# Kernel tuning notes

Measured on AMD Instinct MI355X. Metric: run time of the kernel, lower is better.

Reference implementation:

```python
import jax, jax.numpy as jnp
import numpy as np

B, D, K = 32, 256, 128
DIM, DEPTH, HEADS, MULT, NF = 512, 4, 8, 4, 4
TAU = 0.1
HD = DIM // HEADS  # head_dim = 64


def rms_norm(x, eps=1e-6):
    return x * jax.lax.rsqrt(jnp.mean(x * x, axis=-1, keepdims=True) + eps)


def apply_rope(x, cos, sin):
    # x: (B, S, H, hd); cos/sin: (S, hd//2); interleaved (re, im) pairs
    c = cos[None, :, None, :]
    s = sin[None, :, None, :]
    xr = x[..., 0::2]
    xi = x[..., 1::2]
    out = jnp.stack([xr * c - xi * s, xr * s + xi * c], axis=-1)
    return out.reshape(x.shape)


def one_hot_minus(inputs, shift):
    # (inputs - shift) % K in one-hot space; shift_matrix[u, v] = shift[(v - u) % K]
    Kv = inputs.shape[-1]
    idx = (jnp.arange(Kv)[None, :] - jnp.arange(Kv)[:, None]) % Kv  # (K, K)
    shift_mat = shift[..., idx]  # (..., K, K) axes (u, v)
    return jnp.einsum('...v,...uv->...u', inputs, shift_mat)


def attention(x, qkvW, oW, cos, sin):
    Bx, S, _ = x.shape
    qkv = x @ qkvW.T
    q, k, v = jnp.split(qkv, [HEADS * HD, 2 * HEADS * HD], axis=-1)
    q = rms_norm(q.reshape(Bx, S, HEADS, HD))
    k = rms_norm(k.reshape(Bx, S, HEADS, HD))
    v = v.reshape(Bx, S, HEADS, HD)
    q = apply_rope(q, cos, sin)
    k = apply_rope(k, cos, sin)
    scores = jnp.einsum('bqhd,bkhd->bhqk', q, k) * (1.0 / HD ** 0.5)
    a = jax.nn.softmax(scores, axis=-1)
    o = jnp.einsum('bhqk,bkhd->bqhd', a, v).reshape(Bx, S, DIM)
    return o @ oW.T


def mlp(x, upW, downW):
    h = jax.nn.relu(x @ upW.T)
    return (h * h) @ downW.T


def setup_inputs():
    key = jax.random.key(0)
    ks = jax.random.split(key, 12)
    f = lambda k, sh, sc: jax.random.normal(k, sh, dtype=jnp.float32) * sc
    return {
        'y': jax.random.randint(ks[0], (B, D), 0, K, dtype=jnp.int32),
        'base_logits': f(ks[1], (D, K), 0.02),
        'embed_W': f(ks[2], (NF, DIM, K), 0.05),
        'pos_embed': f(ks[3], (NF, D, DIM), 0.02),
        'qkv_W': f(ks[4], (NF, DEPTH, (HEADS + 2 * HEADS) * HD, DIM), 0.02),
        'out_W': f(ks[5], (NF, DEPTH, DIM, DIM), 0.02),
        'up_W': f(ks[6], (NF, DEPTH, DIM * MULT, DIM), 0.02),
        'down_W': f(ks[7], (NF, DEPTH, DIM, DIM * MULT), 0.02),
        'skip_alpha': jnp.zeros((NF, DEPTH // 2), jnp.float32),
        'head_W': f(ks[8], (NF, K, DIM), 0.02),
        'head_b': jnp.zeros((NF, K), jnp.float32),
    }


def reference(y, base_logits, embed_W, pos_embed, qkv_W, out_W, up_W, down_W,
              skip_alpha, head_W, head_b):
    # RoPE cache over D positions
    dpa = HD // 2
    inv_freq = 1.0 / (10000.0 ** (jnp.arange(dpa, dtype=jnp.float32) / dpa))
    ang = jnp.arange(D, dtype=jnp.float32)[:, None] * inv_freq[None, :]
    cos, sin = jnp.cos(ang), jnp.sin(ang)
    even = (jnp.arange(D) % 2 == 0).astype(jnp.float32)[:, None]  # (D, 1)

    def coupling_net(xin, i):
        h = xin @ embed_W[i].T + pos_embed[i][None]
        mid = DEPTH // 2
        skips = []
        for b in range(DEPTH):
            if mid > 0 and b >= mid:
                h = h + jax.nn.sigmoid(skip_alpha[i, b - mid]) * skips.pop()
            h = h + attention(rms_norm(h), qkv_W[i, b], out_W[i, b], cos, sin)
            h = h + mlp(rms_norm(h), up_W[i, b], down_W[i, b])
            if mid > 0 and b < mid:
                skips.append(h)
        return rms_norm(h) @ head_W[i].T + head_b[i]

    x = jax.nn.one_hot(y, K, dtype=jnp.float32)  # (B, D, K)
    for i in reversed(range(NF)):
        mask = even if i % 2 == 0 else 1.0 - even
        logits = coupling_net(mask * x, i)
        soft = jax.nn.softmax(logits / TAU, axis=-1)
        hard = jax.nn.one_hot(jnp.argmax(logits, axis=-1), K, dtype=jnp.float32)
        loc = soft + jax.lax.stop_gradient(hard - soft)  # straight-through one-hot
        x = mask * x + (1.0 - mask) * one_hot_minus(x, loc)
    log_base = jax.nn.log_softmax(base_logits, axis=-1)
    return jnp.sum(log_base[None] * x, axis=(-1, -2))  # (B,)
```

## Files before the change

kernel.cpp:

```cpp
#include <hip/hip_runtime.h>

typedef __attribute__((ext_vector_type(8))) short s16x8;
typedef __attribute__((ext_vector_type(4))) float f32x4;

#define B_ 32
#define D_ 256
#define K_ 128
#define DIM_ 512
#define HEADS_ 8
#define HD_ 64
#define S_ 256
#define TOK_ (B_*D_)

__device__ __forceinline__ unsigned short f2bf(float f) {
    union { float f; unsigned int u; } v; v.f = f;
    unsigned int r = v.u + 0x7fffu + ((v.u >> 16) & 1u);
    return (unsigned short)(r >> 16);
}
__device__ __forceinline__ float bf2f(unsigned short u) {
    union { unsigned int u; float f; } v; v.u = ((unsigned int)u) << 16;
    return v.f;
}

typedef const __attribute__((address_space(1))) unsigned int* gp1_t;
typedef __attribute__((address_space(3))) unsigned int* lp3_t;
__device__ __forceinline__ void gload16(const void* g, void* l) {
    __builtin_amdgcn_global_load_lds((gp1_t)g, (lp3_t)l, 16, 0, 0);
}

template<int BM, int BN, int EPI, bool SWZ>
__global__ __launch_bounds__(256)
void gemm_p(const unsigned short* __restrict__ A, const unsigned short* __restrict__ Bw,
            void* __restrict__ Cv, const float* __restrict__ bias,
            int K, int ldc, long sA, long sB, int zdiv, long sC1, long sC2)
{
    constexpr int FM = BM/32, FN = BN/32;
    constexpr int AP = BM*4/256, BP = BN*4/256;
    __shared__ unsigned short As[2][BM*32];
    __shared__ unsigned short Bs[2][BN*32];

    const int tid = threadIdx.x;
    const int z = blockIdx.z;
    int bx = blockIdx.x, by = blockIdx.y;
    if constexpr (SWZ) {
        int gx = gridDim.x;
        int nwg = gx * gridDim.y;
        int flat = by*gx + bx;
        int cpx = nwg >> 3;
        int swz = (flat & 7)*cpx + (flat >> 3);
        by = swz / gx; bx = swz - by*gx;
    }
    const long m0 = (long)by * BM;
    const long n0 = (long)bx * BN;
    const unsigned short* Ab = A + z*sA + m0*K;
    const unsigned short* Bb = Bw + z*sB + n0*K;
    const long coff = (long)(z/zdiv)*sC1 + (long)(z%zdiv)*sC2;

    const int w = tid >> 6, lane = tid & 63;
    const int wm = w >> 1, wn = w & 1;
    const int lr = lane & 15, lq = lane >> 4;

    f32x4 acc[FM][FN] = {};

    auto stage = [&](int buf, int k0) {
        #pragma unroll
        for (int p = 0; p < AP; ++p) {
            int idx = p*256 + tid;
            int r = idx >> 2, s = idx & 3;
            int sp = s ^ ((r >> 1) & 3);
            gload16(&Ab[(long)r*K + k0 + sp*8], &As[buf][idx*8]);
        }
        #pragma unroll
        for (int p = 0; p < BP; ++p) {
            int idx = p*256 + tid;
            int r = idx >> 2, s = idx & 3;
            int sp = s ^ ((r >> 1) & 3);
            gload16(&Bb[(long)r*K + k0 + sp*8], &Bs[buf][idx*8]);
        }
    };

    stage(0, 0);
    __syncthreads();
    const int nk = K >> 5;
    for (int t = 0; t < nk; ++t) {
        int cur = t & 1;
        if (t + 1 < nk) stage(cur ^ 1, (t+1) << 5);
        s16x8 af[FM], bfr[FN];
        #pragma unroll
        for (int fm = 0; fm < FM; ++fm) {
            int row = wm*FM*16 + fm*16 + lr;
            af[fm] = *(const s16x8*)&As[cur][row*32 + (lq ^ ((row>>1)&3))*8];
        }
        #pragma unroll
        for (int fn = 0; fn < FN; ++fn) {
            int row = wn*FN*16 + fn*16 + lr;
            bfr[fn] = *(const s16x8*)&Bs[cur][row*32 + (lq ^ ((row>>1)&3))*8];
        }
        #pragma unroll
        for (int fm = 0; fm < FM; ++fm)
            #pragma unroll
            for (int fn = 0; fn < FN; ++fn)
                acc[fm][fn] = __builtin_amdgcn_mfma_f32_16x16x32_bf16(
                    af[fm], bfr[fn], acc[fm][fn], 0, 0, 0);
        __syncthreads();
    }

    #pragma unroll
    for (int fm = 0; fm < FM; ++fm) {
        long mrow = m0 + wm*FM*16 + fm*16 + lq*4;
        #pragma unroll
        for (int fn = 0; fn < FN; ++fn) {
            long ncol = n0 + wn*FN*16 + fn*16 + lr;
            #pragma unroll
            for (int r = 0; r < 4; ++r) {
                long ci = coff + (mrow + r)*ldc + ncol;
                float v = acc[fm][fn][r];
                if constexpr (EPI == 0) ((float*)Cv)[ci] = v;
                else if constexpr (EPI == 1) ((float*)Cv)[ci] += v;
                else if constexpr (EPI == 2) { float t2 = fmaxf(v, 0.f); ((unsigned short*)Cv)[ci] = f2bf(t2*t2); }
                else if constexpr (EPI == 3) ((float*)Cv)[ci] = v + bias[ncol];
                else ((unsigned short*)Cv)[ci] = f2bf(v);
            }
        }
    }
}

__global__ __launch_bounds__(256)
void conv_bf16(const float* __restrict__ in, unsigned short* __restrict__ out, int n4)
{
    for (int i = blockIdx.x*256 + threadIdx.x; i < n4; i += gridDim.x*256) {
        float4 v = ((const float4*)in)[i];
        ushort4 o; o.x = f2bf(v.x); o.y = f2bf(v.y); o.z = f2bf(v.z); o.w = f2bf(v.w);
        ((ushort4*)out)[i] = o;
    }
}

__global__ __launch_bounds__(256)
void attn_scores(const unsigned short* __restrict__ Qn,
                 const unsigned short* __restrict__ Kn,
                 unsigned short* __restrict__ P)
{
    constexpr int KP = 72;
    __shared__ unsigned short Qs[64*KP];
    __shared__ unsigned short Ks[256*KP];
    const int tid = threadIdx.x;
    const int bh = blockIdx.y;
    const int m0 = blockIdx.x * 64;
    const unsigned short* Qb = Qn + (long)bh*S_*HD_ + (long)m0*HD_;
    const unsigned short* Kb = Kn + (long)bh*S_*HD_;

    #pragma unroll
    for (int c = 0; c < 2; ++c) { int lin = c*256 + tid; int row = lin>>3, ko = (lin&7)*8;
        *(int4*)&Qs[row*KP + ko] = *(const int4*)&Qb[row*64 + ko]; }
    #pragma unroll
    for (int c = 0; c < 8; ++c) { int lin = c*256 + tid; int row = lin>>3, ko = (lin&7)*8;
        *(int4*)&Ks[row*KP + ko] = *(const int4*)&Kb[row*64 + ko]; }
    __syncthreads();

    const int w = tid >> 6, lane = tid & 63, lr = lane & 15, lq = lane >> 4;
    s16x8 a0 = *(const s16x8*)&Qs[(w*16 + lr)*KP + lq*8];
    s16x8 a1 = *(const s16x8*)&Qs[(w*16 + lr)*KP + 32 + lq*8];
    f32x4 acc[16];
    #pragma unroll
    for (int fn = 0; fn < 16; ++fn) {
        s16x8 b0 = *(const s16x8*)&Ks[(fn*16 + lr)*KP + lq*8];
        s16x8 b1 = *(const s16x8*)&Ks[(fn*16 + lr)*KP + 32 + lq*8];
        f32x4 c = {0.f, 0.f, 0.f, 0.f};
        c = __builtin_amdgcn_mfma_f32_16x16x32_bf16(a0, b0, c, 0, 0, 0);
        c = __builtin_amdgcn_mfma_f32_16x16x32_bf16(a1, b1, c, 0, 0, 0);
        acc[fn] = c;
    }
    #pragma unroll
    for (int r = 0; r < 4; ++r) {
        float mx = -1e30f;
        #pragma unroll
        for (int fn = 0; fn < 16; ++fn) mx = fmaxf(mx, acc[fn][r]);
        #pragma unroll
        for (int off = 1; off < 16; off <<= 1) mx = fmaxf(mx, __shfl_xor(mx, off, 64));
        float e[16], sum = 0.f;
        #pragma unroll
        for (int fn = 0; fn < 16; ++fn) { e[fn] = __expf(acc[fn][r] - mx); sum += e[fn]; }
        #pragma unroll
        for (int off = 1; off < 16; off <<= 1) sum += __shfl_xor(sum, off, 64);
        float inv = 1.f / sum;
        long rowg = m0 + w*16 + lq*4 + r;
        #pragma unroll
        for (int fn = 0; fn < 16; ++fn)
            P[(long)bh*65536 + rowg*256 + fn*16 + lr] = f2bf(e[fn]*inv);
    }
}

__global__ __launch_bounds__(256)
void rms_rows(const float* __restrict__ in, unsigned short* __restrict__ out)
{
    int row = blockIdx.x*4 + (threadIdx.x >> 6);
    int lane = threadIdx.x & 63;
    const float* r = in + (long)row*DIM_;
    float4 v0 = *(const float4*)&r[lane*4];
    float4 v1 = *(const float4*)&r[256 + lane*4];
    float ss = v0.x*v0.x + v0.y*v0.y + v0.z*v0.z + v0.w*v0.w
             + v1.x*v1.x + v1.y*v1.y + v1.z*v1.z + v1.w*v1.w;
    #pragma unroll
    for (int off = 1; off < 64; off <<= 1) ss += __shfl_xor(ss, off, 64);
    float sc = rsqrtf(ss * (1.f/512.f) + 1e-6f);
    ushort4 o0, o1;
    o0.x = f2bf(v0.x*sc); o0.y = f2bf(v0.y*sc); o0.z = f2bf(v0.z*sc); o0.w = f2bf(v0.w*sc);
    o1.x = f2bf(v1.x*sc); o1.y = f2bf(v1.y*sc); o1.z = f2bf(v1.z*sc); o1.w = f2bf(v1.w*sc);
    *(ushort4*)&out[(long)row*DIM_ + lane*4] = o0;
    *(ushort4*)&out[(long)row*DIM_ + 256 + lane*4] = o1;
}

__global__ __launch_bounds__(256)
void qk_rope(const unsigned short* __restrict__ qkv, const float* __restrict__ cost,
             const float* __restrict__ sint, unsigned short* __restrict__ Qn,
             unsigned short* __restrict__ Kn)
{
    int token = blockIdx.x;
    int s = token & 255;
    int t = threadIdx.x;
    int hh = t >> 5, j = t & 31;
    const unsigned short* row = qkv + (long)token*1536;
    ushort2 qu = *(const ushort2*)&row[hh*64 + 2*j];
    ushort2 ku = *(const ushort2*)&row[512 + hh*64 + 2*j];
    float q0 = bf2f(qu.x), q1 = bf2f(qu.y);
    float k0 = bf2f(ku.x), k1 = bf2f(ku.y);
    float qs = q0*q0 + q1*q1, ks = k0*k0 + k1*k1;
    #pragma unroll
    for (int off = 1; off < 32; off <<= 1) { qs += __shfl_xor(qs, off, 64); ks += __shfl_xor(ks, off, 64); }
    float qsc = rsqrtf(qs*(1.f/64.f) + 1e-6f) * 0.125f;
    float ksc = rsqrtf(ks*(1.f/64.f) + 1e-6f);
    float c = cost[s*32 + j], sn = sint[s*32 + j];
    q0 *= qsc; q1 *= qsc; k0 *= ksc; k1 *= ksc;
    float qo0 = q0*c - q1*sn, qo1 = q0*sn + q1*c;
    float ko0 = k0*c - k1*sn, ko1 = k0*sn + k1*c;
    int bh = (token >> 8)*HEADS_ + hh;
    long base = (long)bh*S_*HD_ + (long)s*HD_ + 2*j;
    ushort2 qw; qw.x = f2bf(qo0); qw.y = f2bf(qo1);
    ushort2 kw; kw.x = f2bf(ko0); kw.y = f2bf(ko1);
    *(ushort2*)&Qn[base] = qw;
    *(ushort2*)&Kn[base] = kw;
}

__global__ __launch_bounds__(256)
void vtrans(const unsigned short* __restrict__ U, unsigned short* __restrict__ VT)
{
    __shared__ unsigned short t[64][65];
    int bh = blockIdx.y, s0 = blockIdx.x*64;
    int b = bh >> 3, h = bh & 7;
    int tid = threadIdx.x;
    #pragma unroll
    for (int p = 0; p < 2; ++p) {
        int lin = p*256 + tid;
        int sr = lin >> 3, dc = (lin & 7)*8;
        *(int4*)&t[sr][dc] = *(const int4*)&U[((long)(b*256 + s0 + sr))*1536 + 1024 + h*64 + dc];
    }
    __syncthreads();
    #pragma unroll
    for (int p = 0; p < 2; ++p) {
        int lin = p*256 + tid;
        int d = lin >> 3, sc = (lin & 7)*8;
        unsigned short tmp[8];
        #pragma unroll
        for (int i = 0; i < 8; ++i) tmp[i] = t[sc + i][d];
        *(int4*)&VT[(long)bh*16384 + (long)d*256 + s0 + sc] = *(const int4*)tmp;
    }
}

__global__ __launch_bounds__(256)
void embed_k(float* __restrict__ h, const int* __restrict__ xidx,
             const float* __restrict__ eW, const float* __restrict__ pos, int par)
{
    int row = blockIdx.x;
    int d = row & 255;
    int mask = (((d & 1) == 0) == (par != 0)) ? 1 : 0;
    int idx = xidx[row];
    int t = threadIdx.x;
    #pragma unroll
    for (int c0 = 0; c0 < 2; ++c0) {
        int c = c0*256 + t;
        float v = pos[d*DIM_ + c];
        if (mask) v += eW[(long)c*K_ + idx];
        h[(long)row*DIM_ + c] = v;
    }
}

__global__ __launch_bounds__(256)
void skip_scale(float* __restrict__ h, const float* __restrict__ alpha, int n4)
{
    float s = 1.f + 1.f/(1.f + __expf(-alpha[0]));
    for (long i = blockIdx.x*256 + threadIdx.x; i < n4; i += (long)gridDim.x*256) {
        float4 v = ((float4*)h)[i];
        v.x *= s; v.y *= s; v.z *= s; v.w *= s;
        ((float4*)h)[i] = v;
    }
}

__global__ __launch_bounds__(256)
void skip_add(float* __restrict__ h, const float* __restrict__ skip,
              const float* __restrict__ alpha, int n4)
{
    float s = 1.f/(1.f + __expf(-alpha[0]));
    for (long i = blockIdx.x*256 + threadIdx.x; i < n4; i += (long)gridDim.x*256) {
        float4 v = ((float4*)h)[i];
        float4 u = ((const float4*)skip)[i];
        v.x += s*u.x; v.y += s*u.y; v.z += s*u.z; v.w += s*u.w;
        ((float4*)h)[i] = v;
    }
}

__global__ __launch_bounds__(256)
void argmax_update(const float* __restrict__ logits, int* __restrict__ xidx, int par)
{
    int row = blockIdx.x*4 + (threadIdx.x >> 6);
    int d = row & 255;
    int maskbit = (((d & 1) == 0) == (par != 0)) ? 1 : 0;
    if (maskbit) return;
    int lane = threadIdx.x & 63;
    float v0 = logits[(long)row*K_ + lane], v1 = logits[(long)row*K_ + 64 + lane];
    float bv; int bi;
    if (v1 > v0) { bv = v1; bi = lane + 64; } else { bv = v0; bi = lane; }
    #pragma unroll
    for (int off = 1; off < 64; off <<= 1) {
        float ov = __shfl_xor(bv, off, 64);
        int oi = __shfl_xor(bi, off, 64);
        if (ov > bv || (ov == bv && oi < bi)) { bv = ov; bi = oi; }
    }
    if (lane == 0) xidx[row] = (xidx[row] - bi) & (K_ - 1);
}

__global__ __launch_bounds__(256)
void setup_cossin(float* __restrict__ cost, float* __restrict__ sint)
{
    for (int idx = blockIdx.x*256 + threadIdx.x; idx < D_*32; idx += gridDim.x*256) {
        int d = idx >> 5, j = idx & 31;
        float inv = powf(10000.f, -(float)j/32.f);
        float ang = (float)d * inv;
        cost[idx] = cosf(ang);
        sint[idx] = sinf(ang);
    }
}

__global__ __launch_bounds__(256)
void setup_lse(const float* __restrict__ bl, float* __restrict__ lse)
{
    int row = blockIdx.x*4 + (threadIdx.x >> 6);
    int lane = threadIdx.x & 63;
    float v0 = bl[(long)row*K_ + lane], v1 = bl[(long)row*K_ + 64 + lane];
    float mx = fmaxf(v0, v1);
    #pragma unroll
    for (int off = 1; off < 64; off <<= 1) mx = fmaxf(mx, __shfl_xor(mx, off, 64));
    float s = __expf(v0 - mx) + __expf(v1 - mx);
    #pragma unroll
    for (int off = 1; off < 64; off <<= 1) s += __shfl_xor(s, off, 64);
    if (lane == 0) lse[row] = logf(s) + mx;
}

__global__ __launch_bounds__(256)
void init_xidx(const int* __restrict__ y, int* __restrict__ xidx)
{
    int i = blockIdx.x*256 + threadIdx.x;
    if (i < TOK_) xidx[i] = y[i];
}

__global__ __launch_bounds__(256)
void final_out(const float* __restrict__ bl, const float* __restrict__ lse,
               const int* __restrict__ xidx, float* __restrict__ out)
{
    int b = blockIdx.x;
    int d = threadIdx.x;
    float v = bl[(long)d*K_ + xidx[b*D_ + d]] - lse[d];
    #pragma unroll
    for (int off = 1; off < 64; off <<= 1) v += __shfl_xor(v, off, 64);
    __shared__ float wsum[4];
    if ((threadIdx.x & 63) == 0) wsum[threadIdx.x >> 6] = v;
    __syncthreads();
    if (threadIdx.x == 0) out[b] = wsum[0] + wsum[1] + wsum[2] + wsum[3];
}

extern "C" void kernel_launch(void* const* d_in, const int* in_sizes, int n_in,
                              void* d_out, int out_size, void* d_ws, size_t ws_size,
                              hipStream_t stream)
{
    const int*   y        = (const int*)  d_in[0];
    const float* base_lg  = (const float*)d_in[1];
    const float* embed_W  = (const float*)d_in[2];
    const float* pos_emb  = (const float*)d_in[3];
    const float* qkv_W    = (const float*)d_in[4];
    const float* out_W    = (const float*)d_in[5];
    const float* up_W     = (const float*)d_in[6];
    const float* down_W   = (const float*)d_in[7];
    const float* skip_al  = (const float*)d_in[8];
    const float* head_W   = (const float*)d_in[9];
    const float* head_b   = (const float*)d_in[10];
    float* out = (float*)d_out;

    char* w = (char*)d_ws;
    auto alloc = [&](size_t bytes) { char* p = w; w += (bytes + 255) & ~(size_t)255; return p; };
    float* cost   = (float*)alloc(D_*32*4);
    float* sint   = (float*)alloc(D_*32*4);
    float* lse    = (float*)alloc(D_*4);
    int*   xidx   = (int*)  alloc(TOK_*4);
    float* h      = (float*)alloc((size_t)TOK_*DIM_*4);
    float* skip   = (float*)alloc((size_t)TOK_*DIM_*4);
    unsigned short* xa = (unsigned short*)alloc((size_t)TOK_*DIM_*2);
    unsigned short* U  = (unsigned short*)alloc((size_t)TOK_*1536*2);
    unsigned short* P  = (unsigned short*)alloc((size_t)256*S_*S_*2);
    unsigned short* Qn = (unsigned short*)alloc((size_t)256*S_*HD_*2);
    unsigned short* Kn = (unsigned short*)alloc((size_t)256*S_*HD_*2);
    unsigned short* VT = (unsigned short*)alloc((size_t)256*S_*HD_*2);
    unsigned short* O  = (unsigned short*)alloc((size_t)TOK_*DIM_*2);
    float* logits = (float*)alloc((size_t)TOK_*K_*4);
    unsigned short* wq = (unsigned short*)alloc((size_t)4*1536*512*2);
    unsigned short* wo = (unsigned short*)alloc((size_t)4*512*512*2);
    unsigned short* wu = (unsigned short*)alloc((size_t)4*2048*512*2);
    unsigned short* wd = (unsigned short*)alloc((size_t)4*512*2048*2);
    unsigned short* wh = (unsigned short*)alloc((size_t)K_*512*2);

    setup_cossin<<<32, 256, 0, stream>>>(cost, sint);
    setup_lse<<<D_/4, 256, 0, stream>>>(base_lg, lse);
    init_xidx<<<TOK_/256, 256, 0, stream>>>(y, xidx);

    const int n4 = TOK_*DIM_/4;

    for (int flow = 3; flow >= 0; --flow) {
        int par = (flow % 2 == 0) ? 1 : 0;

        conv_bf16<<<1024, 256, 0, stream>>>(qkv_W + (long)flow*4*1536*512, wq, 4*1536*512/4);
        conv_bf16<<<1024, 256, 0, stream>>>(out_W + (long)flow*4*512*512,  wo, 4*512*512/4);
        conv_bf16<<<1024, 256, 0, stream>>>(up_W  + (long)flow*4*2048*512, wu, 4*2048*512/4);
        conv_bf16<<<1024, 256, 0, stream>>>(down_W+ (long)flow*4*512*2048, wd, 4*512*2048/4);
        conv_bf16<<<64, 256, 0, stream>>>(head_W + (long)flow*K_*512, wh, K_*512/4);

        embed_k<<<TOK_, 256, 0, stream>>>(h, xidx,
            embed_W + (long)flow*DIM_*K_, pos_emb + (long)flow*D_*DIM_, par);

        for (int layer = 0; layer < 4; ++layer) {
            const unsigned short* qkvW = wq + (long)layer*1536*512;
            const unsigned short* oW   = wo + (long)layer*512*512;
            const unsigned short* upW  = wu + (long)layer*2048*512;
            const unsigned short* dnW  = wd + (long)layer*512*2048;

            if (layer == 2) skip_scale<<<1024, 256, 0, stream>>>(h, skip_al + flow*2 + 0, n4);
            if (layer == 3) skip_add  <<<1024, 256, 0, stream>>>(h, skip, skip_al + flow*2 + 1, n4);

            rms_rows<<<TOK_/4, 256, 0, stream>>>(h, xa);
            gemm_p<128,128,4,true><<<dim3(12,64,1), 256, 0, stream>>>(
                xa, qkvW, U, nullptr, 512, 1536, 0, 0, 1, 0, 0);
            qk_rope<<<TOK_, 256, 0, stream>>>(U, cost, sint, Qn, Kn);
            vtrans<<<dim3(4,256), 256, 0, stream>>>(U, VT);
            attn_scores<<<dim3(4,256), 256, 0, stream>>>(Qn, Kn, P);
            gemm_p<128,64,4,false><<<dim3(1,2,256), 256, 0, stream>>>(
                P, VT, O, nullptr, 256, 512, 65536, 16384, 8, (long)S_*DIM_, 64);
            gemm_p<128,64,1,true><<<dim3(8,64,1), 256, 0, stream>>>(
                O, oW, h, nullptr, 512, 512, 0, 0, 1, 0, 0);

            rms_rows<<<TOK_/4, 256, 0, stream>>>(h, xa);
            gemm_p<128,128,2,true><<<dim3(16,64,1), 256, 0, stream>>>(
                xa, upW, P, nullptr, 512, 2048, 0, 0, 1, 0, 0);
            gemm_p<128,64,1,true><<<dim3(8,64,1), 256, 0, stream>>>(
                P, dnW, h, nullptr, 2048, 512, 0, 0, 1, 0, 0);

            if (layer == 0)
                hipMemcpyAsync(skip, h, (size_t)TOK_*DIM_*4, hipMemcpyDeviceToDevice, stream);
        }

        rms_rows<<<TOK_/4, 256, 0, stream>>>(h, xa);
        gemm_p<64,64,3,true><<<dim3(2,128,1), 256, 0, stream>>>(
            xa, wh, logits, head_b + flow*K_, 512, 128, 0, 0, 1, 0, 0);
        argmax_update<<<TOK_/4, 256, 0, stream>>>(logits, xidx, par);
    }

    final_out<<<B_, 256, 0, stream>>>(base_lg, lse, xidx, out);
}
```

Baseline: 3.060 ms.

## Fuse attention into one kernel, store residual in bf16, shrink GEMM tiles

Fuses the softmax-scores kernel and the P·V GEMM into a single attention kernel that keeps P in swizzled shared memory, so the large bf16 probability matrix never goes to global memory. The residual stream h and the skip buffer move from fp32 to bf16, halving their traffic in rms_rows, the skip kernels and the residual-add GEMM epilogues. GEMM tiles shrink from 128-row to 64-row to raise block count, and the batched-z parameters are dropped. Holding the residual in bf16 adds accumulated rounding error across layers, which can flip argmax decisions.

```diff
diff --git a/kernel.cpp b/kernel.cpp
--- a/kernel.cpp
+++ b/kernel.cpp
@@ -32,7 +32,7 @@
 __global__ __launch_bounds__(256)
 void gemm_p(const unsigned short* __restrict__ A, const unsigned short* __restrict__ Bw,
             void* __restrict__ Cv, const float* __restrict__ bias,
-            int K, int ldc, long sA, long sB, int zdiv, long sC1, long sC2)
+            int K, int ldc)
 {
     constexpr int FM = BM/32, FN = BN/32;
     constexpr int AP = BM*4/256, BP = BN*4/256;
@@ -40,7 +40,6 @@
     __shared__ unsigned short Bs[2][BN*32];
 
     const int tid = threadIdx.x;
-    const int z = blockIdx.z;
     int bx = blockIdx.x, by = blockIdx.y;
     if constexpr (SWZ) {
         int gx = gridDim.x;
@@ -52,9 +51,8 @@
     }
     const long m0 = (long)by * BM;
     const long n0 = (long)bx * BN;
-    const unsigned short* Ab = A + z*sA + m0*K;
-    const unsigned short* Bb = Bw + z*sB + n0*K;
-    const long coff = (long)(z/zdiv)*sC1 + (long)(z%zdiv)*sC2;
+    const unsigned short* Ab = A + m0*K;
+    const unsigned short* Bb = Bw + n0*K;
 
     const int w = tid >> 6, lane = tid & 63;
     const int wm = w >> 1, wn = w & 1;
@@ -113,13 +111,13 @@
             long ncol = n0 + wn*FN*16 + fn*16 + lr;
             #pragma unroll
             for (int r = 0; r < 4; ++r) {
-                long ci = coff + (mrow + r)*ldc + ncol;
+                long ci = (mrow + r)*ldc + ncol;
                 float v = acc[fm][fn][r];
-                if constexpr (EPI == 0) ((float*)Cv)[ci] = v;
-                else if constexpr (EPI == 1) ((float*)Cv)[ci] += v;
-                else if constexpr (EPI == 2) { float t2 = fmaxf(v, 0.f); ((unsigned short*)Cv)[ci] = f2bf(t2*t2); }
+                if constexpr (EPI == 2) { float t2 = fmaxf(v, 0.f); ((unsigned short*)Cv)[ci] = f2bf(t2*t2); }
                 else if constexpr (EPI == 3) ((float*)Cv)[ci] = v + bias[ncol];
-                else ((unsigned short*)Cv)[ci] = f2bf(v);
+                else if constexpr (EPI == 4) ((unsigned short*)Cv)[ci] = f2bf(v);
+                else { unsigned short* cp = (unsigned short*)Cv;
+                       cp[ci] = f2bf(bf2f(cp[ci]) + v); }
             }
         }
     }
@@ -136,40 +134,44 @@
 }
 
 __global__ __launch_bounds__(256)
-void attn_scores(const unsigned short* __restrict__ Qn,
-                 const unsigned short* __restrict__ Kn,
-                 unsigned short* __restrict__ P)
-{
-    constexpr int KP = 72;
-    __shared__ unsigned short Qs[64*KP];
-    __shared__ unsigned short Ks[256*KP];
+void attn_fused(const unsigned short* __restrict__ Qn,
+                const unsigned short* __restrict__ Kn,
+                const unsigned short* __restrict__ VT,
+                unsigned short* __restrict__ O)
+{
+    __shared__ unsigned short Ks[256*64];
+    __shared__ unsigned short Ps[64*256];
     const int tid = threadIdx.x;
     const int bh = blockIdx.y;
     const int m0 = blockIdx.x * 64;
-    const unsigned short* Qb = Qn + (long)bh*S_*HD_ + (long)m0*HD_;
     const unsigned short* Kb = Kn + (long)bh*S_*HD_;
-
-    #pragma unroll
-    for (int c = 0; c < 2; ++c) { int lin = c*256 + tid; int row = lin>>3, ko = (lin&7)*8;
-        *(int4*)&Qs[row*KP + ko] = *(const int4*)&Qb[row*64 + ko]; }
-    #pragma unroll
-    for (int c = 0; c < 8; ++c) { int lin = c*256 + tid; int row = lin>>3, ko = (lin&7)*8;
-        *(int4*)&Ks[row*KP + ko] = *(const int4*)&Kb[row*64 + ko]; }
+    const unsigned short* Vb = VT + (long)bh*S_*HD_;
+
+    #pragma unroll
+    for (int c = 0; c < 8; ++c) {
+        int lin = c*256 + tid;
+        int row = lin >> 3, g = lin & 7;
+        *(int4*)&Ks[row*64 + (g ^ (row & 7))*8] = *(const int4*)&Kb[row*64 + g*8];
+    }
+
+    const int w = tid >> 6, lane = tid & 63, lr = lane & 15, lq = lane >> 4;
+    const unsigned short* Qb = Qn + (long)bh*S_*HD_ + (long)(m0 + w*16 + lr)*HD_;
+    s16x8 a0 = *(const s16x8*)&Qb[lq*8];
+    s16x8 a1 = *(const s16x8*)&Qb[32 + lq*8];
     __syncthreads();
 
-    const int w = tid >> 6, lane = tid & 63, lr = lane & 15, lq = lane >> 4;
-    s16x8 a0 = *(const s16x8*)&Qs[(w*16 + lr)*KP + lq*8];
-    s16x8 a1 = *(const s16x8*)&Qs[(w*16 + lr)*KP + 32 + lq*8];
     f32x4 acc[16];
     #pragma unroll
     for (int fn = 0; fn < 16; ++fn) {
-        s16x8 b0 = *(const s16x8*)&Ks[(fn*16 + lr)*KP + lq*8];
-        s16x8 b1 = *(const s16x8*)&Ks[(fn*16 + lr)*KP + 32 + lq*8];
+        int row = fn*16 + lr;
+        s16x8 b0 = *(const s16x8*)&Ks[row*64 + (lq ^ (row & 7))*8];
+        s16x8 b1 = *(const s16x8*)&Ks[row*64 + ((4 + lq) ^ (row & 7))*8];
         f32x4 c = {0.f, 0.f, 0.f, 0.f};
         c = __builtin_amdgcn_mfma_f32_16x16x32_bf16(a0, b0, c, 0, 0, 0);
         c = __builtin_amdgcn_mfma_f32_16x16x32_bf16(a1, b1, c, 0, 0, 0);
         acc[fn] = c;
     }
+
     #pragma unroll
     for (int r = 0; r < 4; ++r) {
         float mx = -1e30f;
@@ -183,31 +185,55 @@
         #pragma unroll
         for (int off = 1; off < 16; off <<= 1) sum += __shfl_xor(sum, off, 64);
         float inv = 1.f / sum;
-        long rowg = m0 + w*16 + lq*4 + r;
-        #pragma unroll
-        for (int fn = 0; fn < 16; ++fn)
-            P[(long)bh*65536 + rowg*256 + fn*16 + lr] = f2bf(e[fn]*inv);
-    }
-}
-
-__global__ __launch_bounds__(256)
-void rms_rows(const float* __restrict__ in, unsigned short* __restrict__ out)
+        int q = w*16 + lq*4 + r;
+        #pragma unroll
+        for (int fn = 0; fn < 16; ++fn) {
+            int col = fn*16 + lr;
+            Ps[q*256 + ((col >> 3) ^ (q & 7))*8 + (col & 7)] = f2bf(e[fn]*inv);
+        }
+    }
+
+    f32x4 oacc[4] = {};
+    const int q = w*16 + lr;
+    #pragma unroll
+    for (int ks = 0; ks < 8; ++ks) {
+        s16x8 pa = *(const s16x8*)&Ps[q*256 + ((ks*4 + lq) ^ (q & 7))*8];
+        #pragma unroll
+        for (int fn = 0; fn < 4; ++fn) {
+            s16x8 vb = *(const s16x8*)&Vb[(long)(fn*16 + lr)*256 + ks*32 + lq*8];
+            oacc[fn] = __builtin_amdgcn_mfma_f32_16x16x32_bf16(pa, vb, oacc[fn], 0, 0, 0);
+        }
+    }
+
+    int b = bh >> 3, hh = bh & 7;
+    #pragma unroll
+    for (int fn = 0; fn < 4; ++fn) {
+        int d = fn*16 + lr;
+        #pragma unroll
+        for (int r = 0; r < 4; ++r) {
+            int qg = m0 + w*16 + lq*4 + r;
+            O[(long)(b*256 + qg)*DIM_ + hh*64 + d] = f2bf(oacc[fn][r]);
+        }
+    }
+}
+
+__global__ __launch_bounds__(256)
+void rms_rows(const unsigned short* __restrict__ in, unsigned short* __restrict__ out)
 {
     int row = blockIdx.x*4 + (threadIdx.x >> 6);
     int lane = threadIdx.x & 63;
-    const float* r = in + (long)row*DIM_;
-    float4 v0 = *(const float4*)&r[lane*4];
-    float4 v1 = *(const float4*)&r[256 + lane*4];
-    float ss = v0.x*v0.x + v0.y*v0.y + v0.z*v0.z + v0.w*v0.w
-             + v1.x*v1.x + v1.y*v1.y + v1.z*v1.z + v1.w*v1.w;
+    const unsigned short* r = in + (long)row*DIM_ + lane*8;
+    s16x8 v = *(const s16x8*)r;
+    float f[8], ss = 0.f;
+    #pragma unroll
+    for (int i = 0; i < 8; ++i) { f[i] = bf2f((unsigned short)v[i]); ss += f[i]*f[i]; }
     #pragma unroll
     for (int off = 1; off < 64; off <<= 1) ss += __shfl_xor(ss, off, 64);
     float sc = rsqrtf(ss * (1.f/512.f) + 1e-6f);
-    ushort4 o0, o1;
-    o0.x = f2bf(v0.x*sc); o0.y = f2bf(v0.y*sc); o0.z = f2bf(v0.z*sc); o0.w = f2bf(v0.w*sc);
-    o1.x = f2bf(v1.x*sc); o1.y = f2bf(v1.y*sc); o1.z = f2bf(v1.z*sc); o1.w = f2bf(v1.w*sc);
-    *(ushort4*)&out[(long)row*DIM_ + lane*4] = o0;
-    *(ushort4*)&out[(long)row*DIM_ + 256 + lane*4] = o1;
+    unsigned short o[8];
+    #pragma unroll
+    for (int i = 0; i < 8; ++i) o[i] = f2bf(f[i]*sc);
+    *(int4*)&out[(long)row*DIM_ + lane*8] = *(const int4*)o;
 }
 
 __global__ __launch_bounds__(256)
@@ -267,7 +293,7 @@
 }
 
 __global__ __launch_bounds__(256)
-void embed_k(float* __restrict__ h, const int* __restrict__ xidx,
+void embed_k(unsigned short* __restrict__ h, const int* __restrict__ xidx,
              const float* __restrict__ eW, const float* __restrict__ pos, int par)
 {
     int row = blockIdx.x;
@@ -275,36 +301,39 @@
     int mask = (((d & 1) == 0) == (par != 0)) ? 1 : 0;
     int idx = xidx[row];
     int t = threadIdx.x;
-    #pragma unroll
-    for (int c0 = 0; c0 < 2; ++c0) {
-        int c = c0*256 + t;
-        float v = pos[d*DIM_ + c];
-        if (mask) v += eW[(long)c*K_ + idx];
-        h[(long)row*DIM_ + c] = v;
-    }
-}
-
-__global__ __launch_bounds__(256)
-void skip_scale(float* __restrict__ h, const float* __restrict__ alpha, int n4)
+    int c = t*2;
+    float2 p = *(const float2*)&pos[d*DIM_ + c];
+    if (mask) { p.x += eW[(long)c*K_ + idx]; p.y += eW[(long)(c+1)*K_ + idx]; }
+    ushort2 o; o.x = f2bf(p.x); o.y = f2bf(p.y);
+    *(ushort2*)&h[(long)row*DIM_ + c] = o;
+}
+
+__global__ __launch_bounds__(256)
+void skip_scale(unsigned short* __restrict__ h, const float* __restrict__ alpha, int n8)
 {
     float s = 1.f + 1.f/(1.f + __expf(-alpha[0]));
-    for (long i = blockIdx.x*256 + threadIdx.x; i < n4; i += (long)gridDim.x*256) {
-        float4 v = ((float4*)h)[i];
-        v.x *= s; v.y *= s; v.z *= s; v.w *= s;
-        ((float4*)h)[i] = v;
-    }
-}
-
-__global__ __launch_bounds__(256)
-void skip_add(float* __restrict__ h, const float* __restrict__ skip,
-              const float* __restrict__ alpha, int n4)
+    for (int i = blockIdx.x*256 + threadIdx.x; i < n8; i += gridDim.x*256) {
+        s16x8 v = ((s16x8*)h)[i];
+        unsigned short o[8];
+        #pragma unroll
+        for (int j = 0; j < 8; ++j) o[j] = f2bf(bf2f((unsigned short)v[j]) * s);
+        ((int4*)h)[i] = *(const int4*)o;
+    }
+}
+
+__global__ __launch_bounds__(256)
+void skip_add(unsigned short* __restrict__ h, const unsigned short* __restrict__ skip,
+              const float* __restrict__ alpha, int n8)
 {
     float s = 1.f/(1.f + __expf(-alpha[0]));
-    for (long i = blockIdx.x*256 + threadIdx.x; i < n4; i += (long)gridDim.x*256) {
-        float4 v = ((float4*)h)[i];
-        float4 u = ((const float4*)skip)[i];
-        v.x += s*u.x; v.y += s*u.y; v.z += s*u.z; v.w += s*u.w;
-        ((float4*)h)[i] = v;
+    for (int i = blockIdx.x*256 + threadIdx.x; i < n8; i += gridDim.x*256) {
+        s16x8 v = ((s16x8*)h)[i];
+        s16x8 u = ((const s16x8*)skip)[i];
+        unsigned short o[8];
+        #pragma unroll
+        for (int j = 0; j < 8; ++j)
+            o[j] = f2bf(bf2f((unsigned short)v[j]) + s*bf2f((unsigned short)u[j]));
+        ((int4*)h)[i] = *(const int4*)o;
     }
 }
 
@@ -400,15 +429,15 @@
     float* sint   = (float*)alloc(D_*32*4);
     float* lse    = (float*)alloc(D_*4);
     int*   xidx   = (int*)  alloc(TOK_*4);
-    float* h      = (float*)alloc((size_t)TOK_*DIM_*4);
-    float* skip   = (float*)alloc((size_t)TOK_*DIM_*4);
-    unsigned short* xa = (unsigned short*)alloc((size_t)TOK_*DIM_*2);
-    unsigned short* U  = (unsigned short*)alloc((size_t)TOK_*1536*2);
-    unsigned short* P  = (unsigned short*)alloc((size_t)256*S_*S_*2);
-    unsigned short* Qn = (unsigned short*)alloc((size_t)256*S_*HD_*2);
-    unsigned short* Kn = (unsigned short*)alloc((size_t)256*S_*HD_*2);
-    unsigned short* VT = (unsigned short*)alloc((size_t)256*S_*HD_*2);
-    unsigned short* O  = (unsigned short*)alloc((size_t)TOK_*DIM_*2);
+    unsigned short* h    = (unsigned short*)alloc((size_t)TOK_*DIM_*2);
+    unsigned short* skip = (unsigned short*)alloc((size_t)TOK_*DIM_*2);
+    unsigned short* xa   = (unsigned short*)alloc((size_t)TOK_*DIM_*2);
+    unsigned short* U    = (unsigned short*)alloc((size_t)TOK_*1536*2);
+    unsigned short* P    = (unsigned short*)alloc((size_t)TOK_*2048*2);
+    unsigned short* Qn   = (unsigned short*)alloc((size_t)256*S_*HD_*2);
+    unsigned short* Kn   = (unsigned short*)alloc((size_t)256*S_*HD_*2);
+    unsigned short* VT   = (unsigned short*)alloc((size_t)256*S_*HD_*2);
+    unsigned short* O    = (unsigned short*)alloc((size_t)TOK_*DIM_*2);
     float* logits = (float*)alloc((size_t)TOK_*K_*4);
     unsigned short* wq = (unsigned short*)alloc((size_t)4*1536*512*2);
     unsigned short* wo = (unsigned short*)alloc((size_t)4*512*512*2);
@@ -420,7 +449,7 @@
     setup_lse<<<D_/4, 256, 0, stream>>>(base_lg, lse);
     init_xidx<<<TOK_/256, 256, 0, stream>>>(y, xidx);
 
-    const int n4 = TOK_*DIM_/4;
+    const int n8 = TOK_*DIM_/8;
 
     for (int flow = 3; flow >= 0; --flow) {
         int par = (flow % 2 == 0) ? 1 : 0;
@@ -440,33 +469,31 @@
             const unsigned short* upW  = wu + (long)layer*2048*512;
             const unsigned short* dnW  = wd + (long)layer*512*2048;
 
-            if (layer == 2) skip_scale<<<1024, 256, 0, stream>>>(h, skip_al + flow*2 + 0, n4);
-            if (layer == 3) skip_add  <<<1024, 256, 0, stream>>>(h, skip, skip_al + flow*2 + 1, n4);
+            if (layer == 2) skip_scale<<<1024, 256, 0, stream>>>(h, skip_al + flow*2 + 0, n8);
+            if (layer == 3) skip_add  <<<1024, 256, 0, stream>>>(h, skip, skip_al + flow*2 + 1, n8);
 
             rms_rows<<<TOK_/4, 256, 0, stream>>>(h, xa);
-            gemm_p<128,128,4,true><<<dim3(12,64,1), 256, 0, stream>>>(
-                xa, qkvW, U, nullptr, 512, 1536, 0, 0, 1, 0, 0);
+            gemm_p<64,128,4,true><<<dim3(12,128,1), 256, 0, stream>>>(
+                xa, qkvW, U, nullptr, 512, 1536);
             qk_rope<<<TOK_, 256, 0, stream>>>(U, cost, sint, Qn, Kn);
             vtrans<<<dim3(4,256), 256, 0, stream>>>(U, VT);
-            attn_scores<<<dim3(4,256), 256, 0, stream>>>(Qn, Kn, P);
-            gemm_p<128,64,4,false><<<dim3(1,2,256), 256, 0, stream>>>(
-                P, VT, O, nullptr, 256, 512, 65536, 16384, 8, (long)S_*DIM_, 64);
-            gemm_p<128,64,1,true><<<dim3(8,64,1), 256, 0, stream>>>(
-                O, oW, h, nullptr, 512, 512, 0, 0, 1, 0, 0);
+            attn_fused<<<dim3(4,256), 256, 0, stream>>>(Qn, Kn, VT, O);
+            gemm_p<64,64,5,true><<<dim3(8,128,1), 256, 0, stream>>>(
+                O, oW, h, nullptr, 512, 512);
 
             rms_rows<<<TOK_/4, 256, 0, stream>>>(h, xa);
-            gemm_p<128,128,2,true><<<dim3(16,64,1), 256, 0, stream>>>(
-                xa, upW, P, nullptr, 512, 2048, 0, 0, 1, 0, 0);
-            gemm_p<128,64,1,true><<<dim3(8,64,1), 256, 0, stream>>>(
-                P, dnW, h, nullptr, 2048, 512, 0, 0, 1, 0, 0);
+            gemm_p<64,128,2,true><<<dim3(16,128,1), 256, 0, stream>>>(
+                xa, upW, P, nullptr, 512, 2048);
+            gemm_p<64,64,5,true><<<dim3(8,128,1), 256, 0, stream>>>(
+                P, dnW, h, nullptr, 2048, 512);
 
             if (layer == 0)
-                hipMemcpyAsync(skip, h, (size_t)TOK_*DIM_*4, hipMemcpyDeviceToDevice, stream);
+                hipMemcpyAsync(skip, h, (size_t)TOK_*DIM_*2, hipMemcpyDeviceToDevice, stream);
         }
 
         rms_rows<<<TOK_/4, 256, 0, stream>>>(h, xa);
         gemm_p<64,64,3,true><<<dim3(2,128,1), 256, 0, stream>>>(
-            xa, wh, logits, head_b + flow*K_, 512, 128, 0, 0, 1, 0, 0);
+            xa, wh, logits, head_b + flow*K_, 512, 128);
         argmax_update<<<TOK_/4, 256, 0, stream>>>(logits, xidx, par);
     }
 
```

After: 2.859 ms. -6.6%, faster.
